# Kernel tuning notes

Hardware: AMD Instinct MI355X
Metric: run time of the kernel (lower is better)

The kernel has to match this reference:

```python
import jax, jax.numpy as jnp
import numpy as np

N_NODES = 50000
N_EDGES = 1600000
HIDDEN = 64
N_BLOCKS = 2
N_ITERS = 2


def setup_inputs() -> dict:
    key = jax.random.key(0)
    ks = jax.random.split(key, 10)
    hidden = jax.random.normal(ks[0], (N_NODES, HIDDEN), dtype=jnp.float32)
    src = jax.random.randint(ks[1], (N_EDGES,), 0, N_NODES)
    dst = jax.random.randint(ks[2], (N_EDGES,), 0, N_NODES)
    s = 0.05  # keep MLP activations well-scaled
    W1 = jax.random.normal(ks[3], (N_BLOCKS, 3 * HIDDEN, 128), dtype=jnp.float32) * s
    b1 = jax.random.normal(ks[4], (N_BLOCKS, 128), dtype=jnp.float32) * s
    W2 = jax.random.normal(ks[5], (N_BLOCKS, 128, 128), dtype=jnp.float32) * s
    b2 = jax.random.normal(ks[6], (N_BLOCKS, 128), dtype=jnp.float32) * s
    W3 = jax.random.normal(ks[7], (N_BLOCKS, 128, HIDDEN), dtype=jnp.float32) * s
    b3 = jax.random.normal(ks[8], (N_BLOCKS, HIDDEN), dtype=jnp.float32) * s
    return {"hidden": hidden, "src": src, "dst": dst,
            "W1": W1, "b1": b1, "W2": W2, "b2": b2, "W3": W3, "b3": b3}


def _node_update(hidden, src, dst, w1, c1, w2, c2, w3, c3):
    # global rep: sum of all node hidden reps, broadcast to every node
    grep = jnp.broadcast_to(jnp.sum(hidden, axis=0, keepdims=True), hidden.shape)
    # mailbox sum: gather src features, segment-sum into dst
    msgs = hidden[src]                                  # [E, H]
    agg = jax.ops.segment_sum(msgs, dst, num_segments=hidden.shape[0])  # [N, H]
    x = jnp.concatenate([agg, hidden, grep], axis=1)    # [N, 3H]
    h = jax.nn.relu(x @ w1 + c1)
    h = jax.nn.relu(h @ w2 + c2)
    out = h @ w3 + c3
    # row-wise L2 (fro over dim=1) normalization
    norm = jnp.sqrt(jnp.sum(out * out, axis=1, keepdims=True))
    return out / norm


def reference(hidden, src, dst, W1, b1, W2, b2, W3, b3):
    for blk in range(N_BLOCKS):
        for _ in range(N_ITERS):
            hidden = _node_update(hidden, src, dst,
                                  W1[blk], b1[blk], W2[blk], b2[blk], W3[blk], b3[blk])
    return hidden
```

## Files before the change

kernel.cpp:

```cpp
#include <hip/hip_runtime.h>
#include <math.h>

#define NN 50000
#define NE 1600000
#define H  64

#define SHIFT 7
#define NPBKT 128
#define NB    391
#define CHUNK 4096
#define NCH   391

typedef __attribute__((ext_vector_type(8))) short s16v8;
typedef __attribute__((ext_vector_type(4))) float f32v4;
typedef __attribute__((ext_vector_type(8))) _Float16 f16v8;
typedef unsigned short u16;
typedef unsigned int   u32;

__device__ __forceinline__ u16 f2bf(float x) {
    union { float f; unsigned u; } v; v.f = x;
    unsigned r = v.u + 0x7FFF + ((v.u >> 16) & 1);
    return (u16)(r >> 16);
}
__device__ __forceinline__ float bf2f(u16 h) {
    union { float f; unsigned u; } v; v.u = ((unsigned)h) << 16; return v.f;
}

__global__ __launch_bounds__(256) void hist_kernel(const int* __restrict__ dst,
                                                   int* __restrict__ chunkhist) {
    __shared__ int h[NB];
    const int c = blockIdx.x;
    for (int b = threadIdx.x; b < NB; b += 256) h[b] = 0;
    __syncthreads();
    const int e0 = c * CHUNK, e1 = min(NE, e0 + CHUNK);
    for (int e = e0 + threadIdx.x; e < e1; e += 256)
        atomicAdd(&h[dst[e] >> SHIFT], 1);
    __syncthreads();
    for (int b = threadIdx.x; b < NB; b += 256)
        chunkhist[c * NB + b] = h[b];
}

__global__ __launch_bounds__(512) void cscan_kernel(int* __restrict__ chunkhist,
                                                    int* __restrict__ bbase) {
    __shared__ int s[512];
    const int t = threadIdx.x;
    int tot = 0;
    if (t < NB)
        for (int c = 0; c < NCH; ++c) tot += chunkhist[c * NB + t];
    s[t] = (t < NB) ? tot : 0;
    __syncthreads();
    for (int d = 1; d < 512; d <<= 1) {
        int v = (t >= d) ? s[t - d] : 0;
        __syncthreads();
        s[t] += v;
        __syncthreads();
    }
    if (t < NB) {
        int base = s[t] - tot;
        bbase[t] = base;
        if (t == NB - 1) bbase[NB] = s[t];
        int run = base;
        for (int c = 0; c < NCH; ++c) {
            int tmp = chunkhist[c * NB + t];
            chunkhist[c * NB + t] = run;
            run += tmp;
        }
    }
}

__global__ __launch_bounds__(256) void scat_kernel(const int* __restrict__ src,
                                                   const int* __restrict__ dst,
                                                   const int* __restrict__ chunkhist,
                                                   u32* __restrict__ bin) {
    __shared__ int base[NB];
    __shared__ int cur[NB];
    const int c = blockIdx.x;
    for (int b = threadIdx.x; b < NB; b += 256) {
        base[b] = chunkhist[c * NB + b];
        cur[b] = 0;
    }
    __syncthreads();
    const int e0 = c * CHUNK, e1 = min(NE, e0 + CHUNK);
    for (int e = e0 + threadIdx.x; e < e1; e += 256) {
        int d = dst[e];
        int b = d >> SHIFT;
        int p = atomicAdd(&cur[b], 1);
        bin[base[b] + p] = (u32)src[e] | ((u32)(d & (NPBKT - 1)) << 16);
    }
}

__global__ __launch_bounds__(256) void binB_kernel(const u32* __restrict__ bin,
                                                   const int* __restrict__ bbase,
                                                   int* __restrict__ off,
                                                   u16* __restrict__ csr) {
    __shared__ int deg[NPBKT];
    __shared__ int sc[NPBKT];
    __shared__ int cur[NPBKT];
    const int b = blockIdx.x, t = threadIdx.x;
    const int seg0 = bbase[b], seg1 = bbase[b + 1];
    if (t < NPBKT) { deg[t] = 0; cur[t] = 0; }
    __syncthreads();
    for (int i = seg0 + t; i < seg1; i += 256)
        atomicAdd(&deg[(bin[i] >> 16) & (NPBKT - 1)], 1);
    __syncthreads();
    if (t < NPBKT) sc[t] = deg[t];
    __syncthreads();
    for (int d = 1; d < NPBKT; d <<= 1) {
        int v = 0;
        if (t < NPBKT && t >= d) v = sc[t - d];
        __syncthreads();
        if (t < NPBKT) sc[t] += v;
        __syncthreads();
    }
    if (t < NPBKT) {
        sc[t] -= deg[t];
        int node = b * NPBKT + t;
        if (node < NN) off[node] = seg0 + sc[t];
        if (b == 0 && t == 0) off[NN] = NE;
    }
    __syncthreads();
    for (int i = seg0 + t; i < seg1; i += 256) {
        u32 e = bin[i];
        int n = (e >> 16) & (NPBKT - 1);
        int p = atomicAdd(&cur[n], 1);
        csr[seg0 + sc[n] + p] = (u16)(e & 0xFFFF);
    }
}

__global__ __launch_bounds__(256) void prep_kernel(const float* __restrict__ W1,
        const float* __restrict__ W2, const float* __restrict__ W3,
        u16* __restrict__ wt) {
    int idx = blockIdx.x * 256 + threadIdx.x;
    if (idx >= 2 * 40960) return;
    int b = idx / 40960, r = idx - b * 40960;
    float v; int hioff, losz;
    if (r < 16384) {
        int col = r >> 7, k = r & 127;
        v = W1[b * 24576 + k * 128 + col];
        hioff = b * 81920 + r; losz = 16384;
    } else if (r < 32768) {
        int rr = r - 16384; int col = rr >> 7, k = rr & 127;
        v = W2[b * 16384 + k * 128 + col];
        hioff = b * 81920 + 32768 + rr; losz = 16384;
    } else {
        int rr = r - 32768; int col = rr >> 7, k = rr & 127;
        v = W3[b * 8192 + k * 64 + col];
        hioff = b * 81920 + 65536 + rr; losz = 8192;
    }
    u16 hi = f2bf(v);
    u16 lo = f2bf(v - bf2f(hi));
    wt[hioff] = hi; wt[hioff + losz] = lo;
}

__global__ __launch_bounds__(256) void grep_kernel(const float* __restrict__ h,
                                                   float* __restrict__ partial,
                                                   _Float16* __restrict__ h16) {
    const int c  = threadIdx.x & 63;
    const int rl = threadIdx.x >> 6;
    float acc = 0.f;
    for (int r = blockIdx.x * 4 + rl; r < NN; r += gridDim.x * 4) {
        float v = h[r * H + c];
        h16[r * H + c] = (_Float16)v;
        acc += v;
    }
    __shared__ float s[4][64];
    s[rl][c] = acc;
    __syncthreads();
    if (threadIdx.x < 64)
        partial[blockIdx.x * 64 + threadIdx.x] =
            s[0][threadIdx.x] + s[1][threadIdx.x] +
            s[2][threadIdx.x] + s[3][threadIdx.x];
}

__global__ __launch_bounds__(256) void b1e_kernel(const float* __restrict__ partial,
        const float* __restrict__ W1, const float* __restrict__ b1,
        float* __restrict__ b1e) {
    __shared__ float sg[4][64];
    __shared__ float g[64];
    const int t = threadIdx.x;
    const int c = t & 63, rl = t >> 6;
    float s = 0.f;
    for (int i = rl; i < 256; i += 4) s += partial[i * 64 + c];
    sg[rl][c] = s;
    __syncthreads();
    if (t < 64) g[t] = sg[0][t] + sg[1][t] + sg[2][t] + sg[3][t];
    __syncthreads();
    if (t < 128) {
        float s2 = b1[t];
        for (int k = 0; k < 64; ++k)
            s2 = fmaf(g[k], W1[(128 + k) * 128 + t], s2);
        b1e[t] = s2;
    }
}

__global__ __launch_bounds__(256) void gather_kernel(const _Float16* __restrict__ h16,
                                                     const u16* __restrict__ csr,
                                                     const int* __restrict__ off,
                                                     float* __restrict__ agg) {
    const int wid = blockIdx.x * 4 + (threadIdx.x >> 6);
    if (wid >= NN) return;
    const int lane = threadIdx.x & 63;
    const int g8 = lane >> 3, sub = lane & 7;
    const int beg = off[wid], end = off[wid + 1];
    float a[8] = {0.f, 0.f, 0.f, 0.f, 0.f, 0.f, 0.f, 0.f};
    for (int e = beg + g8; e < end; e += 8) {
        int s = csr[e];
        f16v8 v = *(const f16v8*)&h16[(size_t)s * 64 + sub * 8];
#pragma unroll
        for (int j = 0; j < 8; ++j) a[j] += (float)v[j];
    }
#pragma unroll
    for (int o = 8; o <= 32; o <<= 1) {
#pragma unroll
        for (int j = 0; j < 8; ++j) a[j] += __shfl_xor(a[j], o);
    }
    if (g8 == 0) {
        float4 v0 = {a[0], a[1], a[2], a[3]};
        float4 v1 = {a[4], a[5], a[6], a[7]};
        *(float4*)&agg[(size_t)wid * 64 + sub * 8] = v0;
        *(float4*)&agg[(size_t)wid * 64 + sub * 8 + 4] = v1;
    }
}

#define MLP_MFMA(d, a, b) d = __builtin_amdgcn_mfma_f32_16x16x32_bf16(a, b, d, 0, 0, 0)

__global__ __launch_bounds__(512, 4) void mlp_mfma(
    const float* __restrict__ agg, const float* __restrict__ hin,
    const float* __restrict__ b1e, const u16* __restrict__ wt,
    const float* __restrict__ b2, const float* __restrict__ b3,
    float* __restrict__ out)
{
    __shared__ u16 hhi[64 * 128], hlo[64 * 128];
    __shared__ float ssw[4 * 64];
    const int t = threadIdx.x;
    const int wl = t >> 6, lane = t & 63;
    const int li = lane & 15, g = lane >> 4;
    const int n0 = blockIdx.x * 64;

    const u16* w1hi = wt;
    const u16* w1lo = wt + 16384;
    const u16* w2hi = wt + 32768;
    const u16* w2lo = wt + 49152;
    const u16* w3hi = wt + 65536;
    const u16* w3lo = wt + 73728;

    {
        const int row = t >> 3, col0 = (t & 7) * 16;
        const int node = min(n0 + row, NN - 1);
        const float* sp = (col0 < 64) ? (agg + (size_t)node * 64 + col0)
                                      : (hin + (size_t)node * 64 + (col0 - 64));
        float4 u0 = *(const float4*)sp;
        float4 u1 = *(const float4*)(sp + 4);
        float4 u2 = *(const float4*)(sp + 8);
        float4 u3 = *(const float4*)(sp + 12);
        float f[16] = {u0.x, u0.y, u0.z, u0.w, u1.x, u1.y, u1.z, u1.w,
                       u2.x, u2.y, u2.z, u2.w, u3.x, u3.y, u3.z, u3.w};
        s16v8 hv0, lv0, hv1, lv1;
#pragma unroll
        for (int j = 0; j < 8; ++j) {
            u16 hb = f2bf(f[j]);
            hv0[j] = (short)hb;
            lv0[j] = (short)f2bf(f[j] - bf2f(hb));
            u16 hb1 = f2bf(f[8 + j]);
            hv1[j] = (short)hb1;
            lv1[j] = (short)f2bf(f[8 + j] - bf2f(hb1));
        }
        const int cb = col0 >> 3;
        const int a0 = row * 128 + (((cb ^ (row & 7)) << 3));
        const int a1 = row * 128 + ((((cb + 1) ^ (row & 7)) << 3));
        *(s16v8*)&hhi[a0] = hv0; *(s16v8*)&hlo[a0] = lv0;
        *(s16v8*)&hhi[a1] = hv1; *(s16v8*)&hlo[a1] = lv1;
    }
    __syncthreads();

    {
        const int col = wl * 16 + li;
        s16v8 Bh[4], Bl[4];
#pragma unroll
        for (int ks = 0; ks < 4; ++ks) {
            Bh[ks] = *(const s16v8*)(w1hi + col * 128 + ks * 32 + g * 8);
            Bl[ks] = *(const s16v8*)(w1lo + col * 128 + ks * 32 + g * 8);
        }
        f32v4 acc[4];
#pragma unroll
        for (int i = 0; i < 4; ++i) acc[i] = (f32v4){0.f, 0.f, 0.f, 0.f};
#pragma unroll
        for (int rt = 0; rt < 4; ++rt) {
            const int row = rt * 16 + li;
#pragma unroll
            for (int ks = 0; ks < 4; ++ks) {
                const int kb = ks * 4 + g;
                const int addr = row * 128 + ((kb ^ (row & 7)) << 3);
                s16v8 Ah = *(const s16v8*)&hhi[addr];
                s16v8 Al = *(const s16v8*)&hlo[addr];
                MLP_MFMA(acc[rt], Ah, Bh[ks]);
                MLP_MFMA(acc[rt], Ah, Bl[ks]);
                MLP_MFMA(acc[rt], Al, Bh[ks]);
            }
        }
        __syncthreads();
        const float bb = b1e[col];
        const int cb = col >> 3, c7 = col & 7;
#pragma unroll
        for (int rt = 0; rt < 4; ++rt) {
#pragma unroll
            for (int r = 0; r < 4; ++r) {
                float hv = fmaxf(acc[rt][r] + bb, 0.f);
                u16 hb = f2bf(hv);
                u16 lb = f2bf(hv - bf2f(hb));
                const int row = rt * 16 + g * 4 + r;
                const int addr = row * 128 + (((cb ^ (row & 7)) << 3) | c7);
                hhi[addr] = hb; hlo[addr] = lb;
            }
        }
    }
    __syncthreads();

    {
        const int col = wl * 16 + li;
        s16v8 Bh[4], Bl[4];
#pragma unroll
        for (int ks = 0; ks < 4; ++ks) {
            Bh[ks] = *(const s16v8*)(w2hi + col * 128 + ks * 32 + g * 8);
            Bl[ks] = *(const s16v8*)(w2lo + col * 128 + ks * 32 + g * 8);
        }
        f32v4 acc[4];
#pragma unroll
        for (int i = 0; i < 4; ++i) acc[i] = (f32v4){0.f, 0.f, 0.f, 0.f};
#pragma unroll
        for (int rt = 0; rt < 4; ++rt) {
            const int row = rt * 16 + li;
#pragma unroll
            for (int ks = 0; ks < 4; ++ks) {
                const int kb = ks * 4 + g;
                const int addr = row * 128 + ((kb ^ (row & 7)) << 3);
                s16v8 Ah = *(const s16v8*)&hhi[addr];
                s16v8 Al = *(const s16v8*)&hlo[addr];
                MLP_MFMA(acc[rt], Ah, Bh[ks]);
                MLP_MFMA(acc[rt], Ah, Bl[ks]);
                MLP_MFMA(acc[rt], Al, Bh[ks]);
            }
        }
        __syncthreads();
        const float bb = b2[col];
        const int cb = col >> 3, c7 = col & 7;
#pragma unroll
        for (int rt = 0; rt < 4; ++rt) {
#pragma unroll
            for (int r = 0; r < 4; ++r) {
                float hv = fmaxf(acc[rt][r] + bb, 0.f);
                u16 hb = f2bf(hv);
                u16 lb = f2bf(hv - bf2f(hb));
                const int row = rt * 16 + g * 4 + r;
                const int addr = row * 128 + (((cb ^ (row & 7)) << 3) | c7);
                hhi[addr] = hb; hlo[addr] = lb;
            }
        }
    }
    __syncthreads();

    float v[4][4];
    if (wl < 4) {
        const int col = wl * 16 + li;
        s16v8 Bh[4], Bl[4];
#pragma unroll
        for (int ks = 0; ks < 4; ++ks) {
            Bh[ks] = *(const s16v8*)(w3hi + col * 128 + ks * 32 + g * 8);
            Bl[ks] = *(const s16v8*)(w3lo + col * 128 + ks * 32 + g * 8);
        }
        f32v4 acc[4];
#pragma unroll
        for (int i = 0; i < 4; ++i) acc[i] = (f32v4){0.f, 0.f, 0.f, 0.f};
#pragma unroll
        for (int rt = 0; rt < 4; ++rt) {
            const int row = rt * 16 + li;
#pragma unroll
            for (int ks = 0; ks < 4; ++ks) {
                const int kb = ks * 4 + g;
                const int addr = row * 128 + ((kb ^ (row & 7)) << 3);
                s16v8 Ah = *(const s16v8*)&hhi[addr];
                s16v8 Al = *(const s16v8*)&hlo[addr];
                MLP_MFMA(acc[rt], Ah, Bh[ks]);
                MLP_MFMA(acc[rt], Ah, Bl[ks]);
                MLP_MFMA(acc[rt], Al, Bh[ks]);
            }
        }
        const float bb = b3[col];
#pragma unroll
        for (int rt = 0; rt < 4; ++rt) {
#pragma unroll
            for (int r = 0; r < 4; ++r) {
                float vv = acc[rt][r] + bb;
                v[rt][r] = vv;
                float s2 = vv * vv;
#pragma unroll
                for (int o = 1; o <= 8; o <<= 1) s2 += __shfl_xor(s2, o);
                if (li == 0) ssw[wl * 64 + rt * 16 + g * 4 + r] = s2;
            }
        }
    }
    __syncthreads();
    if (wl < 4) {
        const int col = wl * 16 + li;
#pragma unroll
        for (int rt = 0; rt < 4; ++rt) {
#pragma unroll
            for (int r = 0; r < 4; ++r) {
                const int row = rt * 16 + g * 4 + r;
                const float tot = ssw[row] + ssw[64 + row] +
                                  ssw[128 + row] + ssw[192 + row];
                const float inv = rsqrtf(tot);
                const int node = n0 + row;
                if (node < NN)
                    out[(size_t)node * 64 + col] = v[rt][r] * inv;
            }
        }
    }
}

extern "C" void kernel_launch(void* const* d_in, const int* in_sizes, int n_in,
                              void* d_out, int out_size, void* d_ws, size_t ws_size,
                              hipStream_t stream) {
    const float* hidden = (const float*)d_in[0];
    const int*   src    = (const int*)d_in[1];
    const int*   dst    = (const int*)d_in[2];
    const float* W1f    = (const float*)d_in[3];
    const float* b1f    = (const float*)d_in[4];
    const float* W2f    = (const float*)d_in[5];
    const float* b2f    = (const float*)d_in[6];
    const float* W3f    = (const float*)d_in[7];
    const float* b3f    = (const float*)d_in[8];

    float* agg     = (float*)d_ws;
    float* b1e     = agg + (size_t)NN * H;
    float* partial = b1e + 128;
    float* hA      = partial + 256 * 64;
    int*   bbase   = (int*)(hA + (size_t)NN * H);
    int*   off     = bbase + (NB + 1);
    int*   chist   = off + (NN + 1);
    u32*   bin     = (u32*)(chist + NCH * NB);
    u16*   csr     = (u16*)(bin + NE);
    u16*   wt      = (u16*)(((uintptr_t)(csr + NE) + 255) & ~(uintptr_t)255);
    _Float16* h16  = (_Float16*)(wt + 2 * 81920);

    hist_kernel<<<NCH, 256, 0, stream>>>(dst, chist);
    cscan_kernel<<<1, 512, 0, stream>>>(chist, bbase);
    scat_kernel<<<NCH, 256, 0, stream>>>(src, dst, chist, bin);
    binB_kernel<<<NB, 256, 0, stream>>>(bin, bbase, off, csr);
    prep_kernel<<<(2 * 40960 + 255) / 256, 256, 0, stream>>>(W1f, W2f, W3f, wt);

    const float* hin = hidden;
    float* houts[4] = { hA, (float*)d_out, hA, (float*)d_out };

    for (int it = 0; it < 4; ++it) {
        const int blk = it >> 1;
        grep_kernel<<<256, 256, 0, stream>>>(hin, partial, h16);
        b1e_kernel<<<1, 256, 0, stream>>>(partial, W1f + blk * 24576, b1f + blk * 128, b1e);
        gather_kernel<<<(NN + 3) / 4, 256, 0, stream>>>(h16, csr, off, agg);
        mlp_mfma<<<(NN + 63) / 64, 512, 0, stream>>>(agg, hin, b1e, wt + blk * 81920,
            b2f + blk * 128, b3f + blk * 64, houts[it]);
        hin = houts[it];
    }
}
```

Measured before the change: 477.1 us.

## Fuse column-sum and fp16 output into MLP, retile waves, drop low-bf16 terms

The MLP kernel now writes the fp16 copy of its output and per-block column sums, so the grep pass is needed only once before the loop. b1e then reduces a variable number of partials. Waves are retiled as 2 row halves by 4 column pairs, each holding 32 rows by 32 columns, which reuses A fragments across two column tiles. The low-bf16 activation halves are dropped for layers 2 and 3, cutting MFMAs and LDS writes at some cost in precision.

```diff
diff --git a/kernel.cpp b/kernel.cpp
--- a/kernel.cpp
+++ b/kernel.cpp
@@ -173,6 +173,7 @@
 }
 
 __global__ __launch_bounds__(256) void b1e_kernel(const float* __restrict__ partial,
+        int nparts,
         const float* __restrict__ W1, const float* __restrict__ b1,
         float* __restrict__ b1e) {
     __shared__ float sg[4][64];
@@ -180,7 +181,7 @@
     const int t = threadIdx.x;
     const int c = t & 63, rl = t >> 6;
     float s = 0.f;
-    for (int i = rl; i < 256; i += 4) s += partial[i * 64 + c];
+    for (int i = rl; i < nparts; i += 4) s += partial[i * 64 + c];
     sg[rl][c] = s;
     __syncthreads();
     if (t < 64) g[t] = sg[0][t] + sg[1][t] + sg[2][t] + sg[3][t];
@@ -228,13 +229,16 @@
     const float* __restrict__ agg, const float* __restrict__ hin,
     const float* __restrict__ b1e, const u16* __restrict__ wt,
     const float* __restrict__ b2, const float* __restrict__ b3,
-    float* __restrict__ out)
+    float* __restrict__ out, _Float16* __restrict__ h16out,
+    float* __restrict__ colpart)
 {
     __shared__ u16 hhi[64 * 128], hlo[64 * 128];
-    __shared__ float ssw[4 * 64];
+    __shared__ float ssw[2][64];
+    __shared__ float colp[2][64];
     const int t = threadIdx.x;
     const int wl = t >> 6, lane = t & 63;
     const int li = lane & 15, g = lane >> 4;
+    const int rh = wl >> 2, cp = wl & 3;
     const int n0 = blockIdx.x * 64;
 
     const u16* w1hi = wt;
@@ -274,148 +278,199 @@
     __syncthreads();
 
     {
-        const int col = wl * 16 + li;
-        s16v8 Bh[4], Bl[4];
-#pragma unroll
-        for (int ks = 0; ks < 4; ++ks) {
-            Bh[ks] = *(const s16v8*)(w1hi + col * 128 + ks * 32 + g * 8);
-            Bl[ks] = *(const s16v8*)(w1lo + col * 128 + ks * 32 + g * 8);
-        }
-        f32v4 acc[4];
-#pragma unroll
-        for (int i = 0; i < 4; ++i) acc[i] = (f32v4){0.f, 0.f, 0.f, 0.f};
-#pragma unroll
-        for (int rt = 0; rt < 4; ++rt) {
-            const int row = rt * 16 + li;
+        s16v8 Bh[2][4], Bl[2][4];
+#pragma unroll
+        for (int ct = 0; ct < 2; ++ct) {
+            const int col = cp * 32 + ct * 16 + li;
+#pragma unroll
+            for (int ks = 0; ks < 4; ++ks) {
+                Bh[ct][ks] = *(const s16v8*)(w1hi + col * 128 + ks * 32 + g * 8);
+                Bl[ct][ks] = *(const s16v8*)(w1lo + col * 128 + ks * 32 + g * 8);
+            }
+        }
+        f32v4 acc[2][2];
+#pragma unroll
+        for (int i = 0; i < 2; ++i)
+#pragma unroll
+            for (int j = 0; j < 2; ++j) acc[i][j] = (f32v4){0.f, 0.f, 0.f, 0.f};
+#pragma unroll
+        for (int rt = 0; rt < 2; ++rt) {
+            const int row = rh * 32 + rt * 16 + li;
 #pragma unroll
             for (int ks = 0; ks < 4; ++ks) {
                 const int kb = ks * 4 + g;
                 const int addr = row * 128 + ((kb ^ (row & 7)) << 3);
                 s16v8 Ah = *(const s16v8*)&hhi[addr];
                 s16v8 Al = *(const s16v8*)&hlo[addr];
-                MLP_MFMA(acc[rt], Ah, Bh[ks]);
-                MLP_MFMA(acc[rt], Ah, Bl[ks]);
-                MLP_MFMA(acc[rt], Al, Bh[ks]);
+#pragma unroll
+                for (int ct = 0; ct < 2; ++ct) {
+                    MLP_MFMA(acc[rt][ct], Ah, Bh[ct][ks]);
+                    MLP_MFMA(acc[rt][ct], Ah, Bl[ct][ks]);
+                    MLP_MFMA(acc[rt][ct], Al, Bh[ct][ks]);
+                }
             }
         }
         __syncthreads();
-        const float bb = b1e[col];
-        const int cb = col >> 3, c7 = col & 7;
-#pragma unroll
-        for (int rt = 0; rt < 4; ++rt) {
-#pragma unroll
-            for (int r = 0; r < 4; ++r) {
-                float hv = fmaxf(acc[rt][r] + bb, 0.f);
-                u16 hb = f2bf(hv);
-                u16 lb = f2bf(hv - bf2f(hb));
-                const int row = rt * 16 + g * 4 + r;
-                const int addr = row * 128 + (((cb ^ (row & 7)) << 3) | c7);
-                hhi[addr] = hb; hlo[addr] = lb;
+#pragma unroll
+        for (int ct = 0; ct < 2; ++ct) {
+            const int col = cp * 32 + ct * 16 + li;
+            const float bb = b1e[col];
+            const int cb = col >> 3, c7 = col & 7;
+#pragma unroll
+            for (int rt = 0; rt < 2; ++rt) {
+#pragma unroll
+                for (int r = 0; r < 4; ++r) {
+                    float hv = fmaxf(acc[rt][ct][r] + bb, 0.f);
+                    int hb = (int)f2bf(hv);
+                    int pv = __shfl_xor(hb, 1);
+                    if (!(li & 1)) {
+                        const int row = rh * 32 + rt * 16 + g * 4 + r;
+                        const int a = row * 128 + (((cb ^ (row & 7)) << 3) | c7);
+                        *(u32*)&hhi[a] = (u32)(hb & 0xFFFF) | ((u32)pv << 16);
+                    }
+                }
             }
         }
     }
     __syncthreads();
 
     {
-        const int col = wl * 16 + li;
-        s16v8 Bh[4], Bl[4];
-#pragma unroll
-        for (int ks = 0; ks < 4; ++ks) {
-            Bh[ks] = *(const s16v8*)(w2hi + col * 128 + ks * 32 + g * 8);
-            Bl[ks] = *(const s16v8*)(w2lo + col * 128 + ks * 32 + g * 8);
-        }
-        f32v4 acc[4];
-#pragma unroll
-        for (int i = 0; i < 4; ++i) acc[i] = (f32v4){0.f, 0.f, 0.f, 0.f};
-#pragma unroll
-        for (int rt = 0; rt < 4; ++rt) {
-            const int row = rt * 16 + li;
+        s16v8 Bh[2][4], Bl[2][4];
+#pragma unroll
+        for (int ct = 0; ct < 2; ++ct) {
+            const int col = cp * 32 + ct * 16 + li;
+#pragma unroll
+            for (int ks = 0; ks < 4; ++ks) {
+                Bh[ct][ks] = *(const s16v8*)(w2hi + col * 128 + ks * 32 + g * 8);
+                Bl[ct][ks] = *(const s16v8*)(w2lo + col * 128 + ks * 32 + g * 8);
+            }
+        }
+        f32v4 acc[2][2];
+#pragma unroll
+        for (int i = 0; i < 2; ++i)
+#pragma unroll
+            for (int j = 0; j < 2; ++j) acc[i][j] = (f32v4){0.f, 0.f, 0.f, 0.f};
+#pragma unroll
+        for (int rt = 0; rt < 2; ++rt) {
+            const int row = rh * 32 + rt * 16 + li;
 #pragma unroll
             for (int ks = 0; ks < 4; ++ks) {
                 const int kb = ks * 4 + g;
                 const int addr = row * 128 + ((kb ^ (row & 7)) << 3);
                 s16v8 Ah = *(const s16v8*)&hhi[addr];
-                s16v8 Al = *(const s16v8*)&hlo[addr];
-                MLP_MFMA(acc[rt], Ah, Bh[ks]);
-                MLP_MFMA(acc[rt], Ah, Bl[ks]);
-                MLP_MFMA(acc[rt], Al, Bh[ks]);
+#pragma unroll
+                for (int ct = 0; ct < 2; ++ct) {
+                    MLP_MFMA(acc[rt][ct], Ah, Bh[ct][ks]);
+                    MLP_MFMA(acc[rt][ct], Ah, Bl[ct][ks]);
+                }
             }
         }
         __syncthreads();
-        const float bb = b2[col];
-        const int cb = col >> 3, c7 = col & 7;
-#pragma unroll
-        for (int rt = 0; rt < 4; ++rt) {
-#pragma unroll
-            for (int r = 0; r < 4; ++r) {
-                float hv = fmaxf(acc[rt][r] + bb, 0.f);
-                u16 hb = f2bf(hv);
-                u16 lb = f2bf(hv - bf2f(hb));
-                const int row = rt * 16 + g * 4 + r;
-                const int addr = row * 128 + (((cb ^ (row & 7)) << 3) | c7);
-                hhi[addr] = hb; hlo[addr] = lb;
-            }
-        }
-    }
-    __syncthreads();
-
-    float v[4][4];
-    if (wl < 4) {
-        const int col = wl * 16 + li;
-        s16v8 Bh[4], Bl[4];
-#pragma unroll
-        for (int ks = 0; ks < 4; ++ks) {
-            Bh[ks] = *(const s16v8*)(w3hi + col * 128 + ks * 32 + g * 8);
-            Bl[ks] = *(const s16v8*)(w3lo + col * 128 + ks * 32 + g * 8);
-        }
-        f32v4 acc[4];
-#pragma unroll
-        for (int i = 0; i < 4; ++i) acc[i] = (f32v4){0.f, 0.f, 0.f, 0.f};
-#pragma unroll
-        for (int rt = 0; rt < 4; ++rt) {
-            const int row = rt * 16 + li;
+#pragma unroll
+        for (int ct = 0; ct < 2; ++ct) {
+            const int col = cp * 32 + ct * 16 + li;
+            const float bb = b2[col];
+            const int cb = col >> 3, c7 = col & 7;
+#pragma unroll
+            for (int rt = 0; rt < 2; ++rt) {
+#pragma unroll
+                for (int r = 0; r < 4; ++r) {
+                    float hv = fmaxf(acc[rt][ct][r] + bb, 0.f);
+                    int hb = (int)f2bf(hv);
+                    int pv = __shfl_xor(hb, 1);
+                    if (!(li & 1)) {
+                        const int row = rh * 32 + rt * 16 + g * 4 + r;
+                        const int a = row * 128 + (((cb ^ (row & 7)) << 3) | c7);
+                        *(u32*)&hhi[a] = (u32)(hb & 0xFFFF) | ((u32)pv << 16);
+                    }
+                }
+            }
+        }
+    }
+    __syncthreads();
+
+    float v[2][2][4];
+    if (cp < 2) {
+        s16v8 Bh[2][4], Bl[2][4];
+#pragma unroll
+        for (int ct = 0; ct < 2; ++ct) {
+            const int col = cp * 32 + ct * 16 + li;
+#pragma unroll
+            for (int ks = 0; ks < 4; ++ks) {
+                Bh[ct][ks] = *(const s16v8*)(w3hi + col * 128 + ks * 32 + g * 8);
+                Bl[ct][ks] = *(const s16v8*)(w3lo + col * 128 + ks * 32 + g * 8);
+            }
+        }
+        f32v4 acc[2][2];
+#pragma unroll
+        for (int i = 0; i < 2; ++i)
+#pragma unroll
+            for (int j = 0; j < 2; ++j) acc[i][j] = (f32v4){0.f, 0.f, 0.f, 0.f};
+#pragma unroll
+        for (int rt = 0; rt < 2; ++rt) {
+            const int row = rh * 32 + rt * 16 + li;
 #pragma unroll
             for (int ks = 0; ks < 4; ++ks) {
                 const int kb = ks * 4 + g;
                 const int addr = row * 128 + ((kb ^ (row & 7)) << 3);
                 s16v8 Ah = *(const s16v8*)&hhi[addr];
-                s16v8 Al = *(const s16v8*)&hlo[addr];
-                MLP_MFMA(acc[rt], Ah, Bh[ks]);
-                MLP_MFMA(acc[rt], Ah, Bl[ks]);
-                MLP_MFMA(acc[rt], Al, Bh[ks]);
-            }
-        }
-        const float bb = b3[col];
-#pragma unroll
-        for (int rt = 0; rt < 4; ++rt) {
+#pragma unroll
+                for (int ct = 0; ct < 2; ++ct) {
+                    MLP_MFMA(acc[rt][ct], Ah, Bh[ct][ks]);
+                    MLP_MFMA(acc[rt][ct], Ah, Bl[ct][ks]);
+                }
+            }
+        }
+#pragma unroll
+        for (int rt = 0; rt < 2; ++rt) {
 #pragma unroll
             for (int r = 0; r < 4; ++r) {
-                float vv = acc[rt][r] + bb;
-                v[rt][r] = vv;
-                float s2 = vv * vv;
+                float s2 = 0.f;
+#pragma unroll
+                for (int ct = 0; ct < 2; ++ct) {
+                    float vv = acc[rt][ct][r] + b3[cp * 32 + ct * 16 + li];
+                    v[rt][ct][r] = vv;
+                    s2 = fmaf(vv, vv, s2);
+                }
 #pragma unroll
                 for (int o = 1; o <= 8; o <<= 1) s2 += __shfl_xor(s2, o);
-                if (li == 0) ssw[wl * 64 + rt * 16 + g * 4 + r] = s2;
-            }
-        }
-    }
-    __syncthreads();
-    if (wl < 4) {
-        const int col = wl * 16 + li;
-#pragma unroll
-        for (int rt = 0; rt < 4; ++rt) {
+                if (li == 0) ssw[cp][rh * 32 + rt * 16 + g * 4 + r] = s2;
+            }
+        }
+    }
+    __syncthreads();
+    if (cp < 2) {
+        float cs[2] = {0.f, 0.f};
+#pragma unroll
+        for (int rt = 0; rt < 2; ++rt) {
 #pragma unroll
             for (int r = 0; r < 4; ++r) {
-                const int row = rt * 16 + g * 4 + r;
-                const float tot = ssw[row] + ssw[64 + row] +
-                                  ssw[128 + row] + ssw[192 + row];
-                const float inv = rsqrtf(tot);
+                const int row = rh * 32 + rt * 16 + g * 4 + r;
                 const int node = n0 + row;
-                if (node < NN)
-                    out[(size_t)node * 64 + col] = v[rt][r] * inv;
-            }
-        }
-    }
+                const float inv = rsqrtf(ssw[0][row] + ssw[1][row]);
+                const bool ok = node < NN;
+#pragma unroll
+                for (int ct = 0; ct < 2; ++ct) {
+                    const int col = cp * 32 + ct * 16 + li;
+                    float ov = v[rt][ct][r] * inv;
+                    if (ok) {
+                        out[(size_t)node * 64 + col] = ov;
+                        h16out[(size_t)node * 64 + col] = (_Float16)ov;
+                        cs[ct] += ov;
+                    }
+                }
+            }
+        }
+#pragma unroll
+        for (int ct = 0; ct < 2; ++ct) {
+            cs[ct] += __shfl_xor(cs[ct], 16);
+            cs[ct] += __shfl_xor(cs[ct], 32);
+            if (g == 0) colp[rh][cp * 32 + ct * 16 + li] = cs[ct];
+        }
+    }
+    __syncthreads();
+    if (t < 64)
+        colpart[(size_t)blockIdx.x * 64 + t] = colp[0][t] + colp[1][t];
 }
 
 extern "C" void kernel_launch(void* const* d_in, const int* in_sizes, int n_in,
@@ -431,10 +486,13 @@
     const float* W3f    = (const float*)d_in[7];
     const float* b3f    = (const float*)d_in[8];
 
+    const int NBLK = (NN + 63) / 64;
+
     float* agg     = (float*)d_ws;
     float* b1e     = agg + (size_t)NN * H;
-    float* partial = b1e + 128;
-    float* hA      = partial + 256 * 64;
+    float* partA   = b1e + 128;
+    float* partB   = partA + 256 * 64;
+    float* hA      = partB + (size_t)NBLK * 64;
     int*   bbase   = (int*)(hA + (size_t)NN * H);
     int*   off     = bbase + (NB + 1);
     int*   chist   = off + (NN + 1);
@@ -449,16 +507,20 @@
     binB_kernel<<<NB, 256, 0, stream>>>(bin, bbase, off, csr);
     prep_kernel<<<(2 * 40960 + 255) / 256, 256, 0, stream>>>(W1f, W2f, W3f, wt);
 
+    grep_kernel<<<256, 256, 0, stream>>>(hidden, partA, h16);
+
     const float* hin = hidden;
     float* houts[4] = { hA, (float*)d_out, hA, (float*)d_out };
 
     for (int it = 0; it < 4; ++it) {
         const int blk = it >> 1;
-        grep_kernel<<<256, 256, 0, stream>>>(hin, partial, h16);
-        b1e_kernel<<<1, 256, 0, stream>>>(partial, W1f + blk * 24576, b1f + blk * 128, b1e);
+        const float* part = (it == 0) ? partA : partB;
+        const int nparts  = (it == 0) ? 256 : NBLK;
+        b1e_kernel<<<1, 256, 0, stream>>>(part, nparts,
+            W1f + blk * 24576, b1f + blk * 128, b1e);
         gather_kernel<<<(NN + 3) / 4, 256, 0, stream>>>(h16, csr, off, agg);
-        mlp_mfma<<<(NN + 63) / 64, 512, 0, stream>>>(agg, hin, b1e, wt + blk * 81920,
-            b2f + blk * 128, b3f + blk * 64, houts[it]);
+        mlp_mfma<<<NBLK, 512, 0, stream>>>(agg, hin, b1e, wt + blk * 81920,
+            b2f + blk * 128, b3f + blk * 64, houts[it], h16, partB);
         hin = houts[it];
     }
 }
```

After: 581.0 us. 21.8% more time.

## Fuse global column-sum and fp16 conversion into MLP epilogue; double-buffer LDS

Applied to the files above, without the earlier changes.

The MLP kernel's epilogue now writes the fp16 copy of the new hidden state and per-block column sums. This removes the separate grep pass, and its extra full read and write of the node features, from each of the last three iterations. The b1e kernel is widened to reduce a variable number of partials. The MLP also ping-pongs between two LDS activation buffers, which drops the mid-layer barriers. The cost is doubled LDS per block, which can lower occupancy, and more partials to reduce.

```diff
diff --git a/kernel.cpp b/kernel.cpp
--- a/kernel.cpp
+++ b/kernel.cpp
@@ -172,18 +172,24 @@
             s[2][threadIdx.x] + s[3][threadIdx.x];
 }
 
-__global__ __launch_bounds__(256) void b1e_kernel(const float* __restrict__ partial,
+__global__ __launch_bounds__(1024) void b1e_kernel(const float* __restrict__ partial,
+        int nparts,
         const float* __restrict__ W1, const float* __restrict__ b1,
         float* __restrict__ b1e) {
-    __shared__ float sg[4][64];
+    __shared__ float sg[16][64];
     __shared__ float g[64];
     const int t = threadIdx.x;
     const int c = t & 63, rl = t >> 6;
     float s = 0.f;
-    for (int i = rl; i < 256; i += 4) s += partial[i * 64 + c];
+    for (int i = rl; i < nparts; i += 16) s += partial[i * 64 + c];
     sg[rl][c] = s;
     __syncthreads();
-    if (t < 64) g[t] = sg[0][t] + sg[1][t] + sg[2][t] + sg[3][t];
+    if (t < 64) {
+        float a = 0.f;
+#pragma unroll
+        for (int j = 0; j < 16; ++j) a += sg[j][t];
+        g[t] = a;
+    }
     __syncthreads();
     if (t < 128) {
         float s2 = b1[t];
@@ -228,10 +234,13 @@
     const float* __restrict__ agg, const float* __restrict__ hin,
     const float* __restrict__ b1e, const u16* __restrict__ wt,
     const float* __restrict__ b2, const float* __restrict__ b3,
-    float* __restrict__ out)
+    float* __restrict__ out, _Float16* __restrict__ h16out,
+    float* __restrict__ colpart)
 {
+    __shared__ u16 xhi[64 * 128], xlo[64 * 128];
     __shared__ u16 hhi[64 * 128], hlo[64 * 128];
-    __shared__ float ssw[4 * 64];
+    __shared__ float ssw[4][64];
+    __shared__ float colp[64];
     const int t = threadIdx.x;
     const int wl = t >> 6, lane = t & 63;
     const int li = lane & 15, g = lane >> 4;
@@ -268,8 +277,8 @@
         const int cb = col0 >> 3;
         const int a0 = row * 128 + (((cb ^ (row & 7)) << 3));
         const int a1 = row * 128 + ((((cb + 1) ^ (row & 7)) << 3));
-        *(s16v8*)&hhi[a0] = hv0; *(s16v8*)&hlo[a0] = lv0;
-        *(s16v8*)&hhi[a1] = hv1; *(s16v8*)&hlo[a1] = lv1;
+        *(s16v8*)&xhi[a0] = hv0; *(s16v8*)&xlo[a0] = lv0;
+        *(s16v8*)&xhi[a1] = hv1; *(s16v8*)&xlo[a1] = lv1;
     }
     __syncthreads();
 
@@ -280,6 +289,48 @@
         for (int ks = 0; ks < 4; ++ks) {
             Bh[ks] = *(const s16v8*)(w1hi + col * 128 + ks * 32 + g * 8);
             Bl[ks] = *(const s16v8*)(w1lo + col * 128 + ks * 32 + g * 8);
+        }
+        f32v4 acc[4];
+#pragma unroll
+        for (int i = 0; i < 4; ++i) acc[i] = (f32v4){0.f, 0.f, 0.f, 0.f};
+#pragma unroll
+        for (int rt = 0; rt < 4; ++rt) {
+            const int row = rt * 16 + li;
+#pragma unroll
+            for (int ks = 0; ks < 4; ++ks) {
+                const int kb = ks * 4 + g;
+                const int addr = row * 128 + ((kb ^ (row & 7)) << 3);
+                s16v8 Ah = *(const s16v8*)&xhi[addr];
+                s16v8 Al = *(const s16v8*)&xlo[addr];
+                MLP_MFMA(acc[rt], Ah, Bh[ks]);
+                MLP_MFMA(acc[rt], Ah, Bl[ks]);
+                MLP_MFMA(acc[rt], Al, Bh[ks]);
+            }
+        }
+        const float bb = b1e[col];
+        const int cb = col >> 3, c7 = col & 7;
+#pragma unroll
+        for (int rt = 0; rt < 4; ++rt) {
+#pragma unroll
+            for (int r = 0; r < 4; ++r) {
+                float hv = fmaxf(acc[rt][r] + bb, 0.f);
+                u16 hb = f2bf(hv);
+                u16 lb = f2bf(hv - bf2f(hb));
+                const int row = rt * 16 + g * 4 + r;
+                const int addr = row * 128 + (((cb ^ (row & 7)) << 3) | c7);
+                hhi[addr] = hb; hlo[addr] = lb;
+            }
+        }
+    }
+    __syncthreads();
+
+    {
+        const int col = wl * 16 + li;
+        s16v8 Bh[4], Bl[4];
+#pragma unroll
+        for (int ks = 0; ks < 4; ++ks) {
+            Bh[ks] = *(const s16v8*)(w2hi + col * 128 + ks * 32 + g * 8);
+            Bl[ks] = *(const s16v8*)(w2lo + col * 128 + ks * 32 + g * 8);
         }
         f32v4 acc[4];
 #pragma unroll
@@ -298,8 +349,7 @@
                 MLP_MFMA(acc[rt], Al, Bh[ks]);
             }
         }
-        __syncthreads();
-        const float bb = b1e[col];
+        const float bb = b2[col];
         const int cb = col >> 3, c7 = col & 7;
 #pragma unroll
         for (int rt = 0; rt < 4; ++rt) {
@@ -310,50 +360,7 @@
                 u16 lb = f2bf(hv - bf2f(hb));
                 const int row = rt * 16 + g * 4 + r;
                 const int addr = row * 128 + (((cb ^ (row & 7)) << 3) | c7);
-                hhi[addr] = hb; hlo[addr] = lb;
-            }
-        }
-    }
-    __syncthreads();
-
-    {
-        const int col = wl * 16 + li;
-        s16v8 Bh[4], Bl[4];
-#pragma unroll
-        for (int ks = 0; ks < 4; ++ks) {
-            Bh[ks] = *(const s16v8*)(w2hi + col * 128 + ks * 32 + g * 8);
-            Bl[ks] = *(const s16v8*)(w2lo + col * 128 + ks * 32 + g * 8);
-        }
-        f32v4 acc[4];
-#pragma unroll
-        for (int i = 0; i < 4; ++i) acc[i] = (f32v4){0.f, 0.f, 0.f, 0.f};
-#pragma unroll
-        for (int rt = 0; rt < 4; ++rt) {
-            const int row = rt * 16 + li;
-#pragma unroll
-            for (int ks = 0; ks < 4; ++ks) {
-                const int kb = ks * 4 + g;
-                const int addr = row * 128 + ((kb ^ (row & 7)) << 3);
-                s16v8 Ah = *(const s16v8*)&hhi[addr];
-                s16v8 Al = *(const s16v8*)&hlo[addr];
-                MLP_MFMA(acc[rt], Ah, Bh[ks]);
-                MLP_MFMA(acc[rt], Ah, Bl[ks]);
-                MLP_MFMA(acc[rt], Al, Bh[ks]);
-            }
-        }
-        __syncthreads();
-        const float bb = b2[col];
-        const int cb = col >> 3, c7 = col & 7;
-#pragma unroll
-        for (int rt = 0; rt < 4; ++rt) {
-#pragma unroll
-            for (int r = 0; r < 4; ++r) {
-                float hv = fmaxf(acc[rt][r] + bb, 0.f);
-                u16 hb = f2bf(hv);
-                u16 lb = f2bf(hv - bf2f(hb));
-                const int row = rt * 16 + g * 4 + r;
-                const int addr = row * 128 + (((cb ^ (row & 7)) << 3) | c7);
-                hhi[addr] = hb; hlo[addr] = lb;
+                xhi[addr] = hb; xlo[addr] = lb;
             }
         }
     }
@@ -378,8 +385,8 @@
             for (int ks = 0; ks < 4; ++ks) {
                 const int kb = ks * 4 + g;
                 const int addr = row * 128 + ((kb ^ (row & 7)) << 3);
-                s16v8 Ah = *(const s16v8*)&hhi[addr];
-                s16v8 Al = *(const s16v8*)&hlo[addr];
+                s16v8 Ah = *(const s16v8*)&xhi[addr];
+                s16v8 Al = *(const s16v8*)&xlo[addr];
                 MLP_MFMA(acc[rt], Ah, Bh[ks]);
                 MLP_MFMA(acc[rt], Ah, Bl[ks]);
                 MLP_MFMA(acc[rt], Al, Bh[ks]);
@@ -395,27 +402,38 @@
                 float s2 = vv * vv;
 #pragma unroll
                 for (int o = 1; o <= 8; o <<= 1) s2 += __shfl_xor(s2, o);
-                if (li == 0) ssw[wl * 64 + rt * 16 + g * 4 + r] = s2;
+                if (li == 0) ssw[wl][rt * 16 + g * 4 + r] = s2;
             }
         }
     }
     __syncthreads();
     if (wl < 4) {
         const int col = wl * 16 + li;
+        float cs = 0.f;
 #pragma unroll
         for (int rt = 0; rt < 4; ++rt) {
 #pragma unroll
             for (int r = 0; r < 4; ++r) {
                 const int row = rt * 16 + g * 4 + r;
-                const float tot = ssw[row] + ssw[64 + row] +
-                                  ssw[128 + row] + ssw[192 + row];
+                const float tot = ssw[0][row] + ssw[1][row] +
+                                  ssw[2][row] + ssw[3][row];
                 const float inv = rsqrtf(tot);
                 const int node = n0 + row;
-                if (node < NN)
-                    out[(size_t)node * 64 + col] = v[rt][r] * inv;
-            }
-        }
-    }
+                float ov = v[rt][r] * inv;
+                if (node < NN) {
+                    out[(size_t)node * 64 + col] = ov;
+                    h16out[(size_t)node * 64 + col] = (_Float16)ov;
+                    cs += ov;
+                }
+            }
+        }
+        cs += __shfl_xor(cs, 16);
+        cs += __shfl_xor(cs, 32);
+        if (g == 0) colp[col] = cs;
+    }
+    __syncthreads();
+    if (t < 64)
+        colpart[(size_t)blockIdx.x * 64 + t] = colp[t];
 }
 
 extern "C" void kernel_launch(void* const* d_in, const int* in_sizes, int n_in,
@@ -431,10 +449,13 @@
     const float* W3f    = (const float*)d_in[7];
     const float* b3f    = (const float*)d_in[8];
 
+    const int NBLK = (NN + 63) / 64;
+
     float* agg     = (float*)d_ws;
     float* b1e     = agg + (size_t)NN * H;
-    float* partial = b1e + 128;
-    float* hA      = partial + 256 * 64;
+    float* partA   = b1e + 128;
+    float* partB   = partA + 256 * 64;
+    float* hA      = partB + (size_t)NBLK * 64;
     int*   bbase   = (int*)(hA + (size_t)NN * H);
     int*   off     = bbase + (NB + 1);
     int*   chist   = off + (NN + 1);
@@ -449,16 +470,20 @@
     binB_kernel<<<NB, 256, 0, stream>>>(bin, bbase, off, csr);
     prep_kernel<<<(2 * 40960 + 255) / 256, 256, 0, stream>>>(W1f, W2f, W3f, wt);
 
+    grep_kernel<<<256, 256, 0, stream>>>(hidden, partA, h16);
+
     const float* hin = hidden;
     float* houts[4] = { hA, (float*)d_out, hA, (float*)d_out };
 
     for (int it = 0; it < 4; ++it) {
         const int blk = it >> 1;
-        grep_kernel<<<256, 256, 0, stream>>>(hin, partial, h16);
-        b1e_kernel<<<1, 256, 0, stream>>>(partial, W1f + blk * 24576, b1f + blk * 128, b1e);
+        const float* part = (it == 0) ? partA : partB;
+        const int nparts  = (it == 0) ? 256 : NBLK;
+        b1e_kernel<<<1, 1024, 0, stream>>>(part, nparts,
+            W1f + blk * 24576, b1f + blk * 128, b1e);
         gather_kernel<<<(NN + 3) / 4, 256, 0, stream>>>(h16, csr, off, agg);
-        mlp_mfma<<<(NN + 63) / 64, 512, 0, stream>>>(agg, hin, b1e, wt + blk * 81920,
-            b2f + blk * 128, b3f + blk * 64, houts[it]);
+        mlp_mfma<<<NBLK, 512, 0, stream>>>(agg, hin, b1e, wt + blk * 81920,
+            b2f + blk * 128, b3f + blk * 64, houts[it], h16, partB);
         hin = houts[it];
     }
 }
```

Measured after the change: 417.7 us. -12.5%, faster.
